# Kernel tuning notes

Hardware: AMD Instinct MI355X
Metric: run time of the kernel (lower is better)

Reference implementation:

```python
import jax, jax.numpy as jnp
import numpy as np

E, T, D_IN, D_H = 8, 2048, 2048, 5632


def setup_inputs() -> dict:
    key = jax.random.key(0)
    kx, kg, kd, ku = jax.random.split(key, 4)
    scale = 0.02  # init_std-like scaling for weights
    return {
        "x": jax.random.normal(kx, (E, T, D_IN), dtype=jnp.float32),
        "gate_proj": jax.random.normal(kg, (E, D_IN, D_H), dtype=jnp.float32) * scale,
        "down_proj": jax.random.normal(kd, (E, D_IN, D_H), dtype=jnp.float32) * scale,
        "up_proj": jax.random.normal(ku, (E, D_H, D_IN), dtype=jnp.float32) * scale,
        "tokens_per_expert": T,
    }


def reference(x, gate_proj, down_proj, up_proj, tokens_per_expert):
    # ep_size=1: dispatch/combine are identity. Grouped SwiGLU per expert.
    # x: [E, T, d_in]; gate/down: [E, d_in, d_h]; up: [E, d_h, d_in]
    g = jnp.einsum('etd,edh->eth', x, gate_proj)
    u = jnp.einsum('etd,edh->eth', x, down_proj)
    h = jax.nn.silu(g) * u  # [E, T, d_h]
    out = jnp.einsum('eth,ehd->etd', h, up_proj)  # [E, T, d_in]
    return out
```

## Files before the change

kernel.cpp:

```cpp
#include <hip/hip_runtime.h>
#include <hip/hip_bf16.h>


#define NEXP 8
#define TT   2048
#define DIN  2048
#define DH   5632

using short8 = __attribute__((ext_vector_type(8))) short;
using f32x4  = __attribute__((ext_vector_type(4))) float;

static __device__ __forceinline__ float bf2f(unsigned short u) {
    return __uint_as_float(((unsigned int)u) << 16);
}
static __device__ __forceinline__ unsigned short f2bf(float f) {
    unsigned int i = __float_as_uint(f);
    return (unsigned short)((i + 0x7FFFu + ((i >> 16) & 1u)) >> 16);
}
static __device__ __forceinline__ void gld16(const void* g, void* l) {
    __builtin_amdgcn_global_load_lds(
        (const __attribute__((address_space(1))) void*)g,
        (__attribute__((address_space(3))) void*)l, 16, 0, 0);
}

__global__ __launch_bounds__(512, 2) void gemm_gu(
    const unsigned short* __restrict__ Xb,
    const unsigned short* __restrict__ Wgt,
    const unsigned short* __restrict__ Wdt,
    unsigned short* __restrict__ Hb)
{
    __shared__ __align__(16) unsigned short lds[65536];

    const int tid  = threadIdx.x;
    const int wave = tid >> 6, lane = tid & 63;
    const int l15 = lane & 15, l4 = lane >> 4;
    const int wr = wave >> 1, wc = wave & 1;

    const int orig = blockIdx.x;
    const int e    = orig & 7;
    const int w    = orig >> 3;
    const int r32  = w & 31;
    const int m0   = (r32 & 7) * 256;
    const int n0   = ((w >> 5) * 4 + (r32 >> 3)) * 128;

    const int K = DIN, NT = DIN >> 6;

    const unsigned short* A0p = Xb  + (size_t)e * TT * DIN + (size_t)m0 * K;
    const unsigned short* A1p = A0p + (size_t)128 * K;
    const unsigned short* Bgp = Wgt + (size_t)e * DH * DIN + (size_t)n0 * K;
    const unsigned short* Bdp = Wdt + (size_t)e * DH * DIN + (size_t)n0 * K;

    const int c0 = tid, c1 = 512 + tid;
    const int cs0 = c0 ^ ((c0 >> 3) & 7), cs1 = c1 ^ ((c1 >> 3) & 7);
    const int row0 = cs0 >> 3, col0 = (cs0 & 7) * 8;
    const int row1 = cs1 >> 3, col1 = (cs1 & 7) * 8;

    auto stage = [&](const unsigned short* p, int kk, int slot) {
        gld16(p + (size_t)row0 * K + (kk + col0), &lds[slot * 8192 + wave * 512]);
        gld16(p + (size_t)row1 * K + (kk + col1), &lds[slot * 8192 + 4096 + wave * 512]);
    };

    int ibA[4][2], ibB[4][2];
#pragma unroll
    for (int s = 0; s < 4; ++s)
#pragma unroll
        for (int ks = 0; ks < 2; ++ks) {
            const int rA = (wr & 1) * 64 + s * 16 + l15;
            ibA[s][ks] = (rA * 128 + ks * 64 + l4 * 16) ^ ((rA & 7) << 4);
            const int rB = wc * 64 + s * 16 + l15;
            ibB[s][ks] = (rB * 128 + ks * 64 + l4 * 16) ^ ((rB & 7) << 4);
        }
    const int ah = wr >> 1;

    f32x4 accG[4][4] = {}, accU[4][4] = {};
    short8 Aq[4][2], Bq[4][2];

    stage(A0p, 0, 0);  stage(A1p, 0, 1);  stage(Bgp, 0, 2);  stage(Bdp, 0, 3);
    stage(A0p, 64, 4); stage(A1p, 64, 5); stage(Bgp, 64, 6);
    asm volatile("s_waitcnt vmcnt(6)" ::: "memory");
    asm volatile("s_barrier" ::: "memory");

    const char* ldsc = (const char*)lds;
    for (int t = 0; t < NT; ++t) {
        const int sA  = ((4 * t + ah) & 7) * 16384;
        const int sBg = ((4 * t + 2) & 7) * 16384;
        const int sBd = ((4 * t + 3) & 7) * 16384;

#pragma unroll
        for (int s = 0; s < 4; ++s) Aq[s][0] = *(const short8*)(ldsc + sA + ibA[s][0]);
#pragma unroll
        for (int s = 0; s < 4; ++s) Bq[s][0] = *(const short8*)(ldsc + sBg + ibB[s][0]);
        if (t + 1 < NT) stage(Bdp, (t + 1) * 64, (4 * t + 7) & 7);
        asm volatile("s_barrier" ::: "memory");
        asm volatile("s_waitcnt lgkmcnt(0)" ::: "memory");
        __builtin_amdgcn_sched_barrier(0);
        __builtin_amdgcn_s_setprio(1);
#pragma unroll
        for (int m = 0; m < 4; ++m)
#pragma unroll
            for (int n = 0; n < 4; ++n)
                accG[m][n] = __builtin_amdgcn_mfma_f32_16x16x32_bf16(Aq[m][0], Bq[n][0], accG[m][n], 0, 0, 0);
        __builtin_amdgcn_s_setprio(0);
        asm volatile("s_barrier" ::: "memory");

#pragma unroll
        for (int s = 0; s < 4; ++s) Aq[s][1] = *(const short8*)(ldsc + sA + ibA[s][1]);
#pragma unroll
        for (int s = 0; s < 4; ++s) Bq[s][1] = *(const short8*)(ldsc + sBg + ibB[s][1]);
        asm volatile("s_barrier" ::: "memory");
        asm volatile("s_waitcnt lgkmcnt(0)" ::: "memory");
        __builtin_amdgcn_sched_barrier(0);
        __builtin_amdgcn_s_setprio(1);
#pragma unroll
        for (int m = 0; m < 4; ++m)
#pragma unroll
            for (int n = 0; n < 4; ++n)
                accG[m][n] = __builtin_amdgcn_mfma_f32_16x16x32_bf16(Aq[m][1], Bq[n][1], accG[m][n], 0, 0, 0);
        __builtin_amdgcn_s_setprio(0);
        asm volatile("s_barrier" ::: "memory");

#pragma unroll
        for (int s = 0; s < 4; ++s) Bq[s][0] = *(const short8*)(ldsc + sBd + ibB[s][0]);
        if (t + 2 < NT) {
            stage(A0p, (t + 2) * 64, (4 * t + 0) & 7);
            stage(A1p, (t + 2) * 64, (4 * t + 1) & 7);
        }
        asm volatile("s_barrier" ::: "memory");
        asm volatile("s_waitcnt lgkmcnt(0)" ::: "memory");
        __builtin_amdgcn_sched_barrier(0);
        __builtin_amdgcn_s_setprio(1);
#pragma unroll
        for (int m = 0; m < 4; ++m)
#pragma unroll
            for (int n = 0; n < 4; ++n)
                accU[m][n] = __builtin_amdgcn_mfma_f32_16x16x32_bf16(Aq[m][0], Bq[n][0], accU[m][n], 0, 0, 0);
        __builtin_amdgcn_s_setprio(0);
        asm volatile("s_barrier" ::: "memory");

#pragma unroll
        for (int s = 0; s < 4; ++s) Bq[s][1] = *(const short8*)(ldsc + sBd + ibB[s][1]);
        if (t + 2 < NT) stage(Bgp, (t + 2) * 64, (4 * t + 2) & 7);
        asm volatile("s_barrier" ::: "memory");
        asm volatile("s_waitcnt lgkmcnt(0)" ::: "memory");
        __builtin_amdgcn_sched_barrier(0);
        __builtin_amdgcn_s_setprio(1);
#pragma unroll
        for (int m = 0; m < 4; ++m)
#pragma unroll
            for (int n = 0; n < 4; ++n)
                accU[m][n] = __builtin_amdgcn_mfma_f32_16x16x32_bf16(Aq[m][1], Bq[n][1], accU[m][n], 0, 0, 0);
        __builtin_amdgcn_s_setprio(0);
        if (t < NT - 2)       asm volatile("s_waitcnt vmcnt(6)" ::: "memory");
        else if (t == NT - 2) asm volatile("s_waitcnt vmcnt(0)" ::: "memory");
        asm volatile("s_barrier" ::: "memory");
    }

    unsigned short* He = Hb + (size_t)e * TT * DH;
#pragma unroll
    for (int fm = 0; fm < 4; ++fm) {
#pragma unroll
        for (int fn = 0; fn < 4; ++fn) {
            const int col = n0 + wc * 64 + fn * 16 + l15;
#pragma unroll
            for (int j = 0; j < 4; ++j) {
                const int row = m0 + wr * 64 + fm * 16 + l4 * 4 + j;
                const float g = accG[fm][fn][j];
                const float u = accU[fm][fn][j];
                const float h = g / (1.f + __expf(-g)) * u;
                He[(size_t)row * DH + col] = f2bf(h);
            }
        }
    }
}

__global__ __launch_bounds__(512, 2) void gemm_out(
    const unsigned short* __restrict__ Ab,
    const unsigned short* __restrict__ Btb,
    float* __restrict__ Cf)
{
    __shared__ __align__(16) unsigned short lds[65536];

    const int tid  = threadIdx.x;
    const int wave = tid >> 6, lane = tid & 63;
    const int l15 = lane & 15, l4 = lane >> 4;
    const int wr = wave >> 2, wc = wave & 3;

    const int orig = blockIdx.x;
    const int e    = orig & 7;
    const int w    = orig >> 3;
    const int r32  = w & 31;
    const int m0   = (r32 & 7) * 256;
    const int n0   = ((w >> 5) * 4 + (r32 >> 3)) * 256;

    const int M = TT, N = DIN, K = DH, NT = K >> 6;
    const unsigned short* Ae = Ab  + (size_t)e * TT * DH;
    const unsigned short* Be = Btb + (size_t)e * DIN * DH;

    const int c0 = tid, c1 = 512 + tid;
    const int cs0 = c0 ^ ((c0 >> 3) & 7), cs1 = c1 ^ ((c1 >> 3) & 7);
    const int row0 = cs0 >> 3, col0 = (cs0 & 7) * 8;
    const int row1 = cs1 >> 3, col1 = (cs1 & 7) * 8;

    int ibA[4][2], ibB[2][2];
#pragma unroll
    for (int s = 0; s < 4; ++s)
#pragma unroll
        for (int ks = 0; ks < 2; ++ks) {
            const int r = wr * 64 + s * 16 + l15;
            ibA[s][ks] = (r * 128 + ks * 64 + l4 * 16) ^ ((r & 7) << 4);
        }
#pragma unroll
    for (int s = 0; s < 2; ++s)
#pragma unroll
        for (int ks = 0; ks < 2; ++ks) {
            const int r = wc * 32 + s * 16 + l15;
            ibB[s][ks] = (r * 128 + ks * 64 + l4 * 16) ^ ((r & 7) << 4);
        }

    f32x4 acc[8][4] = {};
    short8 Aq[4][2], B0q[2][2], B1q[2][2];

    auto stageA = [&](int ro, int kk, int slot) {
        gld16(Ae + (size_t)(m0 + ro + row0) * K + (kk + col0), &lds[slot * 8192 + wave * 512]);
        gld16(Ae + (size_t)(m0 + ro + row1) * K + (kk + col1), &lds[slot * 8192 + 4096 + wave * 512]);
    };
    auto stageB = [&](int co, int kk, int slot) {
        gld16(Be + (size_t)(n0 + co + row0) * K + (kk + col0), &lds[slot * 8192 + wave * 512]);
        gld16(Be + (size_t)(n0 + co + row1) * K + (kk + col1), &lds[slot * 8192 + 4096 + wave * 512]);
    };

    stageA(0, 0, 0); stageB(0, 0, 1); stageB(128, 0, 2); stageA(128, 0, 3);
    stageA(0, 64, 4); stageB(0, 64, 5); stageB(128, 64, 6);
    asm volatile("s_waitcnt vmcnt(6)" ::: "memory");
    asm volatile("s_barrier" ::: "memory");

    const char* ldsc = (const char*)lds;
    for (int t = 0; t < NT; ++t) {
        const int sA0 = ((4 * t + 0) & 7) * 16384;
        const int sB0 = ((4 * t + 1) & 7) * 16384;
        const int sB1 = ((4 * t + 2) & 7) * 16384;
        const int sA1 = ((4 * t + 3) & 7) * 16384;

#pragma unroll
        for (int s = 0; s < 4; ++s) {
            Aq[s][0] = *(const short8*)(ldsc + sA0 + ibA[s][0]);
            Aq[s][1] = *(const short8*)(ldsc + sA0 + ibA[s][1]);
        }
#pragma unroll
        for (int s = 0; s < 2; ++s) {
            B0q[s][0] = *(const short8*)(ldsc + sB0 + ibB[s][0]);
            B0q[s][1] = *(const short8*)(ldsc + sB0 + ibB[s][1]);
        }
        if (t + 1 < NT) stageA(128, (t + 1) * 64, (4 * t + 7) & 7);
        asm volatile("s_barrier" ::: "memory");
        asm volatile("s_waitcnt lgkmcnt(0)" ::: "memory");
        __builtin_amdgcn_sched_barrier(0);
        __builtin_amdgcn_s_setprio(1);
#pragma unroll
        for (int m = 0; m < 4; ++m)
#pragma unroll
            for (int n = 0; n < 2; ++n) {
                acc[m][n] = __builtin_amdgcn_mfma_f32_16x16x32_bf16(Aq[m][0], B0q[n][0], acc[m][n], 0, 0, 0);
                acc[m][n] = __builtin_amdgcn_mfma_f32_16x16x32_bf16(Aq[m][1], B0q[n][1], acc[m][n], 0, 0, 0);
            }
        __builtin_amdgcn_s_setprio(0);
        asm volatile("s_barrier" ::: "memory");

#pragma unroll
        for (int s = 0; s < 2; ++s) {
            B1q[s][0] = *(const short8*)(ldsc + sB1 + ibB[s][0]);
            B1q[s][1] = *(const short8*)(ldsc + sB1 + ibB[s][1]);
        }
        if (t + 2 < NT) stageA(0, (t + 2) * 64, (4 * t + 8) & 7);
        asm volatile("s_barrier" ::: "memory");
        asm volatile("s_waitcnt lgkmcnt(0)" ::: "memory");
        __builtin_amdgcn_sched_barrier(0);
        __builtin_amdgcn_s_setprio(1);
#pragma unroll
        for (int m = 0; m < 4; ++m)
#pragma unroll
            for (int n = 0; n < 2; ++n) {
                acc[m][2 + n] = __builtin_amdgcn_mfma_f32_16x16x32_bf16(Aq[m][0], B1q[n][0], acc[m][2 + n], 0, 0, 0);
                acc[m][2 + n] = __builtin_amdgcn_mfma_f32_16x16x32_bf16(Aq[m][1], B1q[n][1], acc[m][2 + n], 0, 0, 0);
            }
        __builtin_amdgcn_s_setprio(0);
        asm volatile("s_barrier" ::: "memory");

#pragma unroll
        for (int s = 0; s < 4; ++s) {
            Aq[s][0] = *(const short8*)(ldsc + sA1 + ibA[s][0]);
            Aq[s][1] = *(const short8*)(ldsc + sA1 + ibA[s][1]);
        }
        if (t + 2 < NT) stageB(0, (t + 2) * 64, (4 * t + 9) & 7);
        asm volatile("s_barrier" ::: "memory");
        asm volatile("s_waitcnt lgkmcnt(0)" ::: "memory");
        __builtin_amdgcn_sched_barrier(0);
        __builtin_amdgcn_s_setprio(1);
#pragma unroll
        for (int m = 0; m < 4; ++m)
#pragma unroll
            for (int n = 0; n < 2; ++n) {
                acc[4 + m][2 + n] = __builtin_amdgcn_mfma_f32_16x16x32_bf16(Aq[m][0], B1q[n][0], acc[4 + m][2 + n], 0, 0, 0);
                acc[4 + m][2 + n] = __builtin_amdgcn_mfma_f32_16x16x32_bf16(Aq[m][1], B1q[n][1], acc[4 + m][2 + n], 0, 0, 0);
            }
        __builtin_amdgcn_s_setprio(0);
        asm volatile("s_barrier" ::: "memory");

        if (t + 2 < NT) stageB(128, (t + 2) * 64, (4 * t + 10) & 7);
        asm volatile("s_barrier" ::: "memory");
        __builtin_amdgcn_s_setprio(1);
#pragma unroll
        for (int m = 0; m < 4; ++m)
#pragma unroll
            for (int n = 0; n < 2; ++n) {
                acc[4 + m][n] = __builtin_amdgcn_mfma_f32_16x16x32_bf16(Aq[m][0], B0q[n][0], acc[4 + m][n], 0, 0, 0);
                acc[4 + m][n] = __builtin_amdgcn_mfma_f32_16x16x32_bf16(Aq[m][1], B0q[n][1], acc[4 + m][n], 0, 0, 0);
            }
        __builtin_amdgcn_s_setprio(0);
        if (t < NT - 2)       asm volatile("s_waitcnt vmcnt(6)" ::: "memory");
        else if (t == NT - 2) asm volatile("s_waitcnt vmcnt(0)" ::: "memory");
        asm volatile("s_barrier" ::: "memory");
    }

    float* Ce = Cf + (size_t)e * TT * DIN;
#pragma unroll
    for (int fm = 0; fm < 8; ++fm) {
        const int row_b = (fm >> 2) * 128 + wr * 64 + (fm & 3) * 16 + l4 * 4;
#pragma unroll
        for (int fn = 0; fn < 4; ++fn) {
            const int col = n0 + (fn >> 1) * 128 + wc * 32 + (fn & 1) * 16 + l15;
#pragma unroll
            for (int j = 0; j < 4; ++j)
                Ce[(size_t)(m0 + row_b + j) * N + col] = acc[fm][fn][j];
        }
    }
}

__global__ __launch_bounds__(256) void transpose_f32_bf16(
    const float* __restrict__ in, unsigned short* __restrict__ out,
    int R, int C, size_t ies, size_t oes)
{
    in  += (size_t)blockIdx.z * ies;
    out += (size_t)blockIdx.z * oes;
    __shared__ unsigned short t[64][65];
    const int tid = threadIdx.x;
    const int lr = tid >> 4, lc = (tid & 15) * 4;
    const int r0 = blockIdx.y * 64, c0 = blockIdx.x * 64;
#pragma unroll
    for (int i = 0; i < 4; ++i) {
        const int row = lr + i * 16;
        const float4 v = *(const float4*)(in + (size_t)(r0 + row) * C + c0 + lc);
        t[row][lc + 0] = f2bf(v.x); t[row][lc + 1] = f2bf(v.y);
        t[row][lc + 2] = f2bf(v.z); t[row][lc + 3] = f2bf(v.w);
    }
    __syncthreads();
#pragma unroll
    for (int i = 0; i < 4; ++i) {
        const int crow = lr + i * 16;
        ushort4 wv;
        wv.x = t[lc + 0][crow]; wv.y = t[lc + 1][crow];
        wv.z = t[lc + 2][crow]; wv.w = t[lc + 3][crow];
        *(ushort4*)(out + (size_t)(c0 + crow) * R + r0 + lc) = wv;
    }
}

__global__ __launch_bounds__(256) void conv_f32_bf16(
    const float* __restrict__ in, unsigned short* __restrict__ out, int n4)
{
    int i = blockIdx.x * 256 + threadIdx.x;
    const int stride = gridDim.x * 256;
    for (; i < n4; i += stride) {
        const float4 v = ((const float4*)in)[i];
        ushort4 wv;
        wv.x = f2bf(v.x); wv.y = f2bf(v.y); wv.z = f2bf(v.z); wv.w = f2bf(v.w);
        ((ushort4*)out)[i] = wv;
    }
}

extern "C" void kernel_launch(void* const* d_in, const int* in_sizes, int n_in,
                              void* d_out, int out_size, void* d_ws, size_t ws_size,
                              hipStream_t stream)
{
    const float* x  = (const float*)d_in[0];
    const float* wg = (const float*)d_in[1];
    const float* wd = (const float*)d_in[2];
    const float* wu = (const float*)d_in[3];
    float* out = (float*)d_out;

    const size_t XSZ = (size_t)TT * DIN;
    const size_t WSZ = (size_t)DIN * DH;
    unsigned short* xb  = (unsigned short*)d_ws;
    unsigned short* wgt = xb  + (size_t)NEXP * XSZ;
    unsigned short* wdt = wgt + (size_t)NEXP * WSZ;
    unsigned short* hb  = wdt + (size_t)NEXP * WSZ;

    conv_f32_bf16<<<4096, 256, 0, stream>>>(x, xb, (int)(NEXP * XSZ / 4));
    transpose_f32_bf16<<<dim3(DH / 64, DIN / 64, NEXP), 256, 0, stream>>>(
        wg, wgt, DIN, DH, WSZ, WSZ);
    transpose_f32_bf16<<<dim3(DH / 64, DIN / 64, NEXP), 256, 0, stream>>>(
        wd, wdt, DIN, DH, WSZ, WSZ);
    gemm_gu<<<NEXP * (TT / 256) * (DH / 128), 512, 0, stream>>>(xb, wgt, wdt, hb);
    transpose_f32_bf16<<<dim3(DIN / 64, DH / 64, NEXP), 256, 0, stream>>>(
        wu, wgt, DH, DIN, WSZ, WSZ);
    gemm_out<<<NEXP * (TT / 256) * (DIN / 256), 512, 0, stream>>>(hb, wgt, out);
}
```

Before: 1.283 ms.

## Remap gate/up GEMM waves to 2x4 grid with full-K per A-half phase

Reorganizes the fused gate/down GEMM so each wave covers 64 rows by 32 columns in each of the two 128-row A halves (2x4 wave grid instead of 4x2). Each phase now loads a whole 64-wide K slice of one operand and issues both K sub-steps of MFMAs back to back. The fourth phase reuses fragments already in registers, so it needs no LDS read. The goal is fewer LDS fragment reads per MFMA and a different global-to-LDS staging order, at the cost of changed register pressure and a new slot rotation that must stay race-free.

Measured after the change: 1.259 ms. About the same (-1.9%).

```diff
diff --git a/kernel.cpp b/kernel.cpp
--- a/kernel.cpp
+++ b/kernel.cpp
@@ -34,7 +34,7 @@
     const int tid  = threadIdx.x;
     const int wave = tid >> 6, lane = tid & 63;
     const int l15 = lane & 15, l4 = lane >> 4;
-    const int wr = wave >> 1, wc = wave & 1;
+    const int wr = wave >> 2, wc = wave & 3;
 
     const int orig = blockIdx.x;
     const int e    = orig & 7;
@@ -45,110 +45,130 @@
 
     const int K = DIN, NT = DIN >> 6;
 
-    const unsigned short* A0p = Xb  + (size_t)e * TT * DIN + (size_t)m0 * K;
-    const unsigned short* A1p = A0p + (size_t)128 * K;
-    const unsigned short* Bgp = Wgt + (size_t)e * DH * DIN + (size_t)n0 * K;
-    const unsigned short* Bdp = Wdt + (size_t)e * DH * DIN + (size_t)n0 * K;
+    const unsigned short* Ae = Xb  + (size_t)e * TT * DIN;
+    const unsigned short* Gp = Wgt + (size_t)e * DH * DIN + (size_t)n0 * K;
+    const unsigned short* Dp = Wdt + (size_t)e * DH * DIN + (size_t)n0 * K;
 
     const int c0 = tid, c1 = 512 + tid;
     const int cs0 = c0 ^ ((c0 >> 3) & 7), cs1 = c1 ^ ((c1 >> 3) & 7);
     const int row0 = cs0 >> 3, col0 = (cs0 & 7) * 8;
     const int row1 = cs1 >> 3, col1 = (cs1 & 7) * 8;
 
-    auto stage = [&](const unsigned short* p, int kk, int slot) {
+    int ibA[4][2], ibB[2][2];
+#pragma unroll
+    for (int s = 0; s < 4; ++s)
+#pragma unroll
+        for (int ks = 0; ks < 2; ++ks) {
+            const int r = wr * 64 + s * 16 + l15;
+            ibA[s][ks] = (r * 128 + ks * 64 + l4 * 16) ^ ((r & 7) << 4);
+        }
+#pragma unroll
+    for (int s = 0; s < 2; ++s)
+#pragma unroll
+        for (int ks = 0; ks < 2; ++ks) {
+            const int r = wc * 32 + s * 16 + l15;
+            ibB[s][ks] = (r * 128 + ks * 64 + l4 * 16) ^ ((r & 7) << 4);
+        }
+
+    f32x4 acc[8][4] = {};
+    short8 Aq[4][2], Gq[2][2], Dq[2][2];
+
+    auto stageA = [&](int ro, int kk, int slot) {
+        gld16(Ae + (size_t)(m0 + ro + row0) * K + (kk + col0), &lds[slot * 8192 + wave * 512]);
+        gld16(Ae + (size_t)(m0 + ro + row1) * K + (kk + col1), &lds[slot * 8192 + 4096 + wave * 512]);
+    };
+    auto stageW = [&](const unsigned short* p, int kk, int slot) {
         gld16(p + (size_t)row0 * K + (kk + col0), &lds[slot * 8192 + wave * 512]);
         gld16(p + (size_t)row1 * K + (kk + col1), &lds[slot * 8192 + 4096 + wave * 512]);
     };
 
-    int ibA[4][2], ibB[4][2];
-#pragma unroll
-    for (int s = 0; s < 4; ++s)
-#pragma unroll
-        for (int ks = 0; ks < 2; ++ks) {
-            const int rA = (wr & 1) * 64 + s * 16 + l15;
-            ibA[s][ks] = (rA * 128 + ks * 64 + l4 * 16) ^ ((rA & 7) << 4);
-            const int rB = wc * 64 + s * 16 + l15;
-            ibB[s][ks] = (rB * 128 + ks * 64 + l4 * 16) ^ ((rB & 7) << 4);
-        }
-    const int ah = wr >> 1;
-
-    f32x4 accG[4][4] = {}, accU[4][4] = {};
-    short8 Aq[4][2], Bq[4][2];
-
-    stage(A0p, 0, 0);  stage(A1p, 0, 1);  stage(Bgp, 0, 2);  stage(Bdp, 0, 3);
-    stage(A0p, 64, 4); stage(A1p, 64, 5); stage(Bgp, 64, 6);
+    stageA(0, 0, 0);  stageW(Gp, 0, 1);  stageW(Dp, 0, 2);  stageA(128, 0, 3);
+    stageA(0, 64, 4); stageW(Gp, 64, 5); stageW(Dp, 64, 6);
     asm volatile("s_waitcnt vmcnt(6)" ::: "memory");
     asm volatile("s_barrier" ::: "memory");
 
     const char* ldsc = (const char*)lds;
     for (int t = 0; t < NT; ++t) {
-        const int sA  = ((4 * t + ah) & 7) * 16384;
-        const int sBg = ((4 * t + 2) & 7) * 16384;
-        const int sBd = ((4 * t + 3) & 7) * 16384;
-
-#pragma unroll
-        for (int s = 0; s < 4; ++s) Aq[s][0] = *(const short8*)(ldsc + sA + ibA[s][0]);
-#pragma unroll
-        for (int s = 0; s < 4; ++s) Bq[s][0] = *(const short8*)(ldsc + sBg + ibB[s][0]);
-        if (t + 1 < NT) stage(Bdp, (t + 1) * 64, (4 * t + 7) & 7);
-        asm volatile("s_barrier" ::: "memory");
-        asm volatile("s_waitcnt lgkmcnt(0)" ::: "memory");
-        __builtin_amdgcn_sched_barrier(0);
-        __builtin_amdgcn_s_setprio(1);
-#pragma unroll
-        for (int m = 0; m < 4; ++m)
-#pragma unroll
-            for (int n = 0; n < 4; ++n)
-                accG[m][n] = __builtin_amdgcn_mfma_f32_16x16x32_bf16(Aq[m][0], Bq[n][0], accG[m][n], 0, 0, 0);
-        __builtin_amdgcn_s_setprio(0);
-        asm volatile("s_barrier" ::: "memory");
-
-#pragma unroll
-        for (int s = 0; s < 4; ++s) Aq[s][1] = *(const short8*)(ldsc + sA + ibA[s][1]);
-#pragma unroll
-        for (int s = 0; s < 4; ++s) Bq[s][1] = *(const short8*)(ldsc + sBg + ibB[s][1]);
-        asm volatile("s_barrier" ::: "memory");
-        asm volatile("s_waitcnt lgkmcnt(0)" ::: "memory");
-        __builtin_amdgcn_sched_barrier(0);
-        __builtin_amdgcn_s_setprio(1);
-#pragma unroll
-        for (int m = 0; m < 4; ++m)
-#pragma unroll
-            for (int n = 0; n < 4; ++n)
-                accG[m][n] = __builtin_amdgcn_mfma_f32_16x16x32_bf16(Aq[m][1], Bq[n][1], accG[m][n], 0, 0, 0);
-        __builtin_amdgcn_s_setprio(0);
-        asm volatile("s_barrier" ::: "memory");
-
-#pragma unroll
-        for (int s = 0; s < 4; ++s) Bq[s][0] = *(const short8*)(ldsc + sBd + ibB[s][0]);
-        if (t + 2 < NT) {
-            stage(A0p, (t + 2) * 64, (4 * t + 0) & 7);
-            stage(A1p, (t + 2) * 64, (4 * t + 1) & 7);
-        }
-        asm volatile("s_barrier" ::: "memory");
-        asm volatile("s_waitcnt lgkmcnt(0)" ::: "memory");
-        __builtin_amdgcn_sched_barrier(0);
-        __builtin_amdgcn_s_setprio(1);
-#pragma unroll
-        for (int m = 0; m < 4; ++m)
-#pragma unroll
-            for (int n = 0; n < 4; ++n)
-                accU[m][n] = __builtin_amdgcn_mfma_f32_16x16x32_bf16(Aq[m][0], Bq[n][0], accU[m][n], 0, 0, 0);
-        __builtin_amdgcn_s_setprio(0);
-        asm volatile("s_barrier" ::: "memory");
-
-#pragma unroll
-        for (int s = 0; s < 4; ++s) Bq[s][1] = *(const short8*)(ldsc + sBd + ibB[s][1]);
-        if (t + 2 < NT) stage(Bgp, (t + 2) * 64, (4 * t + 2) & 7);
-        asm volatile("s_barrier" ::: "memory");
-        asm volatile("s_waitcnt lgkmcnt(0)" ::: "memory");
-        __builtin_amdgcn_sched_barrier(0);
-        __builtin_amdgcn_s_setprio(1);
-#pragma unroll
-        for (int m = 0; m < 4; ++m)
-#pragma unroll
-            for (int n = 0; n < 4; ++n)
-                accU[m][n] = __builtin_amdgcn_mfma_f32_16x16x32_bf16(Aq[m][1], Bq[n][1], accU[m][n], 0, 0, 0);
+        const int sA0 = ((4 * t + 0) & 7) * 16384;
+        const int sG  = ((4 * t + 1) & 7) * 16384;
+        const int sD  = ((4 * t + 2) & 7) * 16384;
+        const int sA1 = ((4 * t + 3) & 7) * 16384;
+
+#pragma unroll
+        for (int s = 0; s < 4; ++s) {
+            Aq[s][0] = *(const short8*)(ldsc + sA0 + ibA[s][0]);
+            Aq[s][1] = *(const short8*)(ldsc + sA0 + ibA[s][1]);
+        }
+#pragma unroll
+        for (int s = 0; s < 2; ++s) {
+            Gq[s][0] = *(const short8*)(ldsc + sG + ibB[s][0]);
+            Gq[s][1] = *(const short8*)(ldsc + sG + ibB[s][1]);
+        }
+        if (t + 1 < NT) stageA(128, (t + 1) * 64, (4 * t + 7) & 7);
+        asm volatile("s_barrier" ::: "memory");
+        asm volatile("s_waitcnt lgkmcnt(0)" ::: "memory");
+        __builtin_amdgcn_sched_barrier(0);
+        __builtin_amdgcn_s_setprio(1);
+#pragma unroll
+        for (int m = 0; m < 4; ++m)
+#pragma unroll
+            for (int n = 0; n < 2; ++n) {
+                acc[m][n] = __builtin_amdgcn_mfma_f32_16x16x32_bf16(Aq[m][0], Gq[n][0], acc[m][n], 0, 0, 0);
+                acc[m][n] = __builtin_amdgcn_mfma_f32_16x16x32_bf16(Aq[m][1], Gq[n][1], acc[m][n], 0, 0, 0);
+            }
+        __builtin_amdgcn_s_setprio(0);
+        asm volatile("s_barrier" ::: "memory");
+
+#pragma unroll
+        for (int s = 0; s < 2; ++s) {
+            Dq[s][0] = *(const short8*)(ldsc + sD + ibB[s][0]);
+            Dq[s][1] = *(const short8*)(ldsc + sD + ibB[s][1]);
+        }
+        if (t + 2 < NT) stageA(0, (t + 2) * 64, (4 * t + 8) & 7);
+        asm volatile("s_barrier" ::: "memory");
+        asm volatile("s_waitcnt lgkmcnt(0)" ::: "memory");
+        __builtin_amdgcn_sched_barrier(0);
+        __builtin_amdgcn_s_setprio(1);
+#pragma unroll
+        for (int m = 0; m < 4; ++m)
+#pragma unroll
+            for (int n = 0; n < 2; ++n) {
+                acc[m][2 + n] = __builtin_amdgcn_mfma_f32_16x16x32_bf16(Aq[m][0], Dq[n][0], acc[m][2 + n], 0, 0, 0);
+                acc[m][2 + n] = __builtin_amdgcn_mfma_f32_16x16x32_bf16(Aq[m][1], Dq[n][1], acc[m][2 + n], 0, 0, 0);
+            }
+        __builtin_amdgcn_s_setprio(0);
+        asm volatile("s_barrier" ::: "memory");
+
+#pragma unroll
+        for (int s = 0; s < 4; ++s) {
+            Aq[s][0] = *(const short8*)(ldsc + sA1 + ibA[s][0]);
+            Aq[s][1] = *(const short8*)(ldsc + sA1 + ibA[s][1]);
+        }
+        if (t + 2 < NT) stageW(Gp, (t + 2) * 64, (4 * t + 9) & 7);
+        asm volatile("s_barrier" ::: "memory");
+        asm volatile("s_waitcnt lgkmcnt(0)" ::: "memory");
+        __builtin_amdgcn_sched_barrier(0);
+        __builtin_amdgcn_s_setprio(1);
+#pragma unroll
+        for (int m = 0; m < 4; ++m)
+#pragma unroll
+            for (int n = 0; n < 2; ++n) {
+                acc[4 + m][2 + n] = __builtin_amdgcn_mfma_f32_16x16x32_bf16(Aq[m][0], Dq[n][0], acc[4 + m][2 + n], 0, 0, 0);
+                acc[4 + m][2 + n] = __builtin_amdgcn_mfma_f32_16x16x32_bf16(Aq[m][1], Dq[n][1], acc[4 + m][2 + n], 0, 0, 0);
+            }
+        __builtin_amdgcn_s_setprio(0);
+        asm volatile("s_barrier" ::: "memory");
+
+        if (t + 2 < NT) stageW(Dp, (t + 2) * 64, (4 * t + 10) & 7);
+        asm volatile("s_barrier" ::: "memory");
+        __builtin_amdgcn_s_setprio(1);
+#pragma unroll
+        for (int m = 0; m < 4; ++m)
+#pragma unroll
+            for (int n = 0; n < 2; ++n) {
+                acc[4 + m][n] = __builtin_amdgcn_mfma_f32_16x16x32_bf16(Aq[m][0], Gq[n][0], acc[4 + m][n], 0, 0, 0);
+                acc[4 + m][n] = __builtin_amdgcn_mfma_f32_16x16x32_bf16(Aq[m][1], Gq[n][1], acc[4 + m][n], 0, 0, 0);
+            }
         __builtin_amdgcn_s_setprio(0);
         if (t < NT - 2)       asm volatile("s_waitcnt vmcnt(6)" ::: "memory");
         else if (t == NT - 2) asm volatile("s_waitcnt vmcnt(0)" ::: "memory");
@@ -157,17 +177,17 @@
 
     unsigned short* He = Hb + (size_t)e * TT * DH;
 #pragma unroll
-    for (int fm = 0; fm < 4; ++fm) {
-#pragma unroll
-        for (int fn = 0; fn < 4; ++fn) {
-            const int col = n0 + wc * 64 + fn * 16 + l15;
+    for (int fm = 0; fm < 8; ++fm) {
+        const int row_b = m0 + (fm >> 2) * 128 + wr * 64 + (fm & 3) * 16 + l4 * 4;
+#pragma unroll
+        for (int nr = 0; nr < 2; ++nr) {
+            const int col = n0 + wc * 32 + nr * 16 + l15;
 #pragma unroll
             for (int j = 0; j < 4; ++j) {
-                const int row = m0 + wr * 64 + fm * 16 + l4 * 4 + j;
-                const float g = accG[fm][fn][j];
-                const float u = accU[fm][fn][j];
+                const float g = acc[fm][nr][j];
+                const float u = acc[fm][2 + nr][j];
                 const float h = g / (1.f + __expf(-g)) * u;
-                He[(size_t)row * DH + col] = f2bf(h);
+                He[(size_t)(row_b + j) * DH + col] = f2bf(h);
             }
         }
     }
```
